# Kernel optimization log

Measured on AMD Instinct MI355X. Metric: run time of the kernel, lower is better.

Reference implementation:

```python
import jax, jax.numpy as jnp
import numpy as np

B, C, H, W = 32, 512, 64, 64
K = 32  # num_codes


def setup_inputs() -> dict:
    key = jax.random.key(0)
    k1, k2, k3 = jax.random.split(key, 3)
    x = jax.random.normal(k1, (B, C, H, W), dtype=jnp.float32)
    std = 1.0 / (K * C) ** 0.5
    codewords = jax.random.uniform(k2, (K, C), dtype=jnp.float32, minval=-std, maxval=std)
    scale = jax.random.uniform(k3, (K,), dtype=jnp.float32, minval=-1.0, maxval=0.0)
    return {"x": x, "codewords": codewords, "scale": scale}


def reference(x, codewords, scale):
    # x: [B, C, H, W] -> [B, N, C] with N = H*W
    b, c = x.shape[0], x.shape[1]
    xf = x.reshape(b, c, -1).transpose(0, 2, 1)  # [B, N, C]
    # scaled L2: scale_k * ||x_n - c_k||^2, expanded algebraically to avoid [B,N,K,C]
    x2 = jnp.sum(xf * xf, axis=-1)                      # [B, N]
    c2 = jnp.sum(codewords * codewords, axis=-1)        # [K]
    xc = jnp.einsum('bnc,kc->bnk', xf, codewords)       # [B, N, K]
    dist = scale[None, None, :] * (x2[:, :, None] - 2.0 * xc + c2[None, None, :])
    w = jax.nn.softmax(dist, axis=2)                    # [B, N, K]
    # aggregate: sum_n w_{nk} * (x_n - c_k) = (w^T x) - (sum_n w_{nk}) * c_k
    wx = jnp.einsum('bnk,bnc->bkc', w, xf)              # [B, K, C]
    wsum = jnp.sum(w, axis=1)                           # [B, K]
    encoded_feat = wx - wsum[:, :, None] * codewords[None, :, :]  # [B, K, C]
    return encoded_feat
```

## Files before the change

kernel.cpp:

```cpp
#include <hip/hip_runtime.h>
#include <hip/hip_bf16.h>
#include <stdint.h>

#define Bdim 32
#define Cdim 512
#define Ndim 4096
#define Kdim 32
#define NCHUNK 32
#define NCHUNKS 8
#define PBLK 16

static constexpr size_t WS_WSUM_OFF = (size_t)512 * Kdim * Cdim * 4;
static constexpr size_t WS_C2_OFF   = WS_WSUM_OFF + (size_t)512 * Kdim * 4;

typedef __fp16 hf2 __attribute__((ext_vector_type(2)));
typedef _Float16 ff2 __attribute__((ext_vector_type(2)));

static __device__ __forceinline__ float dot2f(hf2 a, hf2 b, float c) {
#if __has_builtin(__builtin_amdgcn_fdot2)
    return __builtin_amdgcn_fdot2(__builtin_bit_cast(ff2, a),
                                  __builtin_bit_cast(ff2, b), c, false);
#else
    return c + (float)a[0] * (float)b[0] + (float)a[1] * (float)b[1];
#endif
}

__global__ __launch_bounds__(256) void k0_c2(const float* __restrict__ cw,
                                             float* __restrict__ c2) {
    __shared__ float partl[8][32];
    int t = threadIdx.x;
    int k = t & 31, g = t >> 5;
    float s = 0.f;
    int c0 = g * 64;
    for (int c = c0; c < c0 + 64; ++c) {
        float v = cw[k * Cdim + c];
        s += v * v;
    }
    partl[g][k] = s;
    __syncthreads();
    if (t < 32) {
        float tot = 0.f;
        #pragma unroll
        for (int gg = 0; gg < 8; ++gg) tot += partl[gg][t];
        c2[t] = tot;
    }
}

__global__ __launch_bounds__(256, 2) void k1_fused(const float* __restrict__ x,
                                                   const float* __restrict__ cw,
                                                   const float* __restrict__ scale,
                                                   const float* __restrict__ c2g,
                                                   float* __restrict__ part,
                                                   float* __restrict__ wsum_part) {
    __shared__ hf2   xh[NCHUNK][260];
    __shared__ hf2   cwh[Kdim][256];
    __shared__ float w_s[NCHUNK][36];
    __shared__ float x2_s[NCHUNK];

    const int t   = threadIdx.x;
    const int blk = blockIdx.x;
    const int b   = blk >> 4;
    const int p   = blk & 15;

    const int n1 = t & 31;
    const int kq = t >> 5;
    const int q   = t & 7;
    const int cc0 = t >> 3;
    const int cg = t & 63;
    const int kh = t >> 6;

    float sc[4], cc2[4];
    #pragma unroll
    for (int j = 0; j < 4; ++j) {
        sc[j]  = scale[4 * kq + j];
        cc2[j] = c2g[4 * kq + j];
    }

    if (t < NCHUNK) x2_s[t] = 0.f;
    #pragma unroll
    for (int i = 0; i < 16; ++i) {
        int f4 = t + 256 * i;
        int k  = f4 >> 7;
        int c4 = f4 & 127;
        float4 v = *(const float4*)(cw + (size_t)k * Cdim + 4 * c4);
        cwh[k][2 * c4 + 0] = __builtin_amdgcn_cvt_pkrtz(v.x, v.y);
        cwh[k][2 * c4 + 1] = __builtin_amdgcn_cvt_pkrtz(v.z, v.w);
    }

    float acc[8][8];
    #pragma unroll
    for (int a = 0; a < 8; ++a)
        #pragma unroll
        for (int d = 0; d < 8; ++d) acc[a][d] = 0.f;
    float wsum_r = 0.f;

    const float* xb = x + (size_t)b * Cdim * Ndim + p * (NCHUNKS * NCHUNK);
    __syncthreads();

    for (int ci = 0; ci < NCHUNKS; ++ci) {
        const int n0 = ci * NCHUNK;

        float x2p[4] = {0.f, 0.f, 0.f, 0.f};
        #pragma unroll
        for (int it = 0; it < 8; ++it) {
            int cc = cc0 + 32 * it;
            const float* r0 = xb + (size_t)(2 * cc) * Ndim + n0 + 4 * q;
            float4 a  = *(const float4*)r0;
            float4 bb = *(const float4*)(r0 + Ndim);
            xh[4 * q + 0][cc] = __builtin_amdgcn_cvt_pkrtz(a.x, bb.x);
            xh[4 * q + 1][cc] = __builtin_amdgcn_cvt_pkrtz(a.y, bb.y);
            xh[4 * q + 2][cc] = __builtin_amdgcn_cvt_pkrtz(a.z, bb.z);
            xh[4 * q + 3][cc] = __builtin_amdgcn_cvt_pkrtz(a.w, bb.w);
            x2p[0] += a.x * a.x + bb.x * bb.x;
            x2p[1] += a.y * a.y + bb.y * bb.y;
            x2p[2] += a.z * a.z + bb.z * bb.z;
            x2p[3] += a.w * a.w + bb.w * bb.w;
        }
        #pragma unroll
        for (int j = 0; j < 4; ++j) {
            float v = x2p[j];
            v += __shfl_xor(v, 8);
            v += __shfl_xor(v, 16);
            v += __shfl_xor(v, 32);
            if ((t & 56) == 0) atomicAdd(&x2_s[4 * q + j], v);
        }
        __syncthreads();

        {
            const int k0 = 4 * kq;
            float d0 = 0.f, d1 = 0.f, d2 = 0.f, d3 = 0.f;
            #pragma unroll 4
            for (int cp = 0; cp < 64; ++cp) {
                uint4 xu = *(const uint4*)&xh[n1][4 * cp];
                hf2 x0 = __builtin_bit_cast(hf2, xu.x);
                hf2 x1 = __builtin_bit_cast(hf2, xu.y);
                hf2 x2v = __builtin_bit_cast(hf2, xu.z);
                hf2 x3 = __builtin_bit_cast(hf2, xu.w);
                uint4 cu0 = *(const uint4*)&cwh[k0 + 0][4 * cp];
                uint4 cu1 = *(const uint4*)&cwh[k0 + 1][4 * cp];
                uint4 cu2 = *(const uint4*)&cwh[k0 + 2][4 * cp];
                uint4 cu3 = *(const uint4*)&cwh[k0 + 3][4 * cp];
                d0 = dot2f(x0, __builtin_bit_cast(hf2, cu0.x), d0);
                d0 = dot2f(x1, __builtin_bit_cast(hf2, cu0.y), d0);
                d0 = dot2f(x2v, __builtin_bit_cast(hf2, cu0.z), d0);
                d0 = dot2f(x3, __builtin_bit_cast(hf2, cu0.w), d0);
                d1 = dot2f(x0, __builtin_bit_cast(hf2, cu1.x), d1);
                d1 = dot2f(x1, __builtin_bit_cast(hf2, cu1.y), d1);
                d1 = dot2f(x2v, __builtin_bit_cast(hf2, cu1.z), d1);
                d1 = dot2f(x3, __builtin_bit_cast(hf2, cu1.w), d1);
                d2 = dot2f(x0, __builtin_bit_cast(hf2, cu2.x), d2);
                d2 = dot2f(x1, __builtin_bit_cast(hf2, cu2.y), d2);
                d2 = dot2f(x2v, __builtin_bit_cast(hf2, cu2.z), d2);
                d2 = dot2f(x3, __builtin_bit_cast(hf2, cu2.w), d2);
                d3 = dot2f(x0, __builtin_bit_cast(hf2, cu3.x), d3);
                d3 = dot2f(x1, __builtin_bit_cast(hf2, cu3.y), d3);
                d3 = dot2f(x2v, __builtin_bit_cast(hf2, cu3.z), d3);
                d3 = dot2f(x3, __builtin_bit_cast(hf2, cu3.w), d3);
            }
            float xx = x2_s[n1];
            w_s[n1][k0 + 0] = sc[0] * (xx - 2.f * d0 + cc2[0]);
            w_s[n1][k0 + 1] = sc[1] * (xx - 2.f * d1 + cc2[1]);
            w_s[n1][k0 + 2] = sc[2] * (xx - 2.f * d2 + cc2[2]);
            w_s[n1][k0 + 3] = sc[3] * (xx - 2.f * d3 + cc2[3]);
        }
        __syncthreads();

        if (t < 32) {
            float v[32];
            float m = -3.4e38f;
            #pragma unroll
            for (int k = 0; k < 32; ++k) {
                v[k] = w_s[t][k];
                m = fmaxf(m, v[k]);
            }
            float s = 0.f;
            #pragma unroll
            for (int k = 0; k < 32; ++k) {
                v[k] = __expf(v[k] - m);
                s += v[k];
            }
            float inv = 1.f / s;
            #pragma unroll
            for (int k = 0; k < 32; ++k) w_s[t][k] = v[k] * inv;
        }
        __syncthreads();

        {
            const int k0 = 8 * kh;
            #pragma unroll 4
            for (int n = 0; n < NCHUNK; ++n) {
                uint4 xu = *(const uint4*)&xh[n][4 * cg];
                hf2 h0 = __builtin_bit_cast(hf2, xu.x);
                hf2 h1 = __builtin_bit_cast(hf2, xu.y);
                hf2 h2 = __builtin_bit_cast(hf2, xu.z);
                hf2 h3 = __builtin_bit_cast(hf2, xu.w);
                float xf[8];
                xf[0] = (float)h0[0]; xf[1] = (float)h0[1];
                xf[2] = (float)h1[0]; xf[3] = (float)h1[1];
                xf[4] = (float)h2[0]; xf[5] = (float)h2[1];
                xf[6] = (float)h3[0]; xf[7] = (float)h3[1];
                float4 wa = *(const float4*)&w_s[n][k0];
                float4 wb = *(const float4*)&w_s[n][k0 + 4];
                float wv[8] = {wa.x, wa.y, wa.z, wa.w, wb.x, wb.y, wb.z, wb.w};
                #pragma unroll
                for (int kk = 0; kk < 8; ++kk)
                    #pragma unroll
                    for (int j = 0; j < 8; ++j)
                        acc[kk][j] += wv[kk] * xf[j];
            }
        }
        if (t < 32) {
            float s = 0.f;
            #pragma unroll 4
            for (int n = 0; n < NCHUNK; ++n) s += w_s[n][t];
            wsum_r += s;
        } else if (t < 64) {
            x2_s[t - 32] = 0.f;
        }
        __syncthreads();
    }

    {
        const int k0 = 8 * kh;
        float* pb = part + (size_t)blk * (Kdim * Cdim);
        #pragma unroll
        for (int kk = 0; kk < 8; ++kk) {
            float4 v0 = make_float4(acc[kk][0], acc[kk][1], acc[kk][2], acc[kk][3]);
            float4 v1 = make_float4(acc[kk][4], acc[kk][5], acc[kk][6], acc[kk][7]);
            float* op = pb + (size_t)(k0 + kk) * Cdim + 8 * cg;
            *(float4*)op = v0;
            *(float4*)(op + 4) = v1;
        }
        if (t < 32) wsum_part[blk * Kdim + t] = wsum_r;
    }
}

__global__ __launch_bounds__(256) void k2_reduce(const float* __restrict__ part,
                                                 const float* __restrict__ wsum_part,
                                                 const float* __restrict__ cw,
                                                 float* __restrict__ out) {
    int blk = blockIdx.x;
    int b = blk >> 5, k = blk & 31;
    int t = threadIdx.x;
    float ws = 0.f;
    #pragma unroll
    for (int p = 0; p < PBLK; ++p) ws += wsum_part[(b * PBLK + p) * Kdim + k];
    int c = 2 * t;
    float sx = 0.f, sy = 0.f;
    #pragma unroll
    for (int p = 0; p < PBLK; ++p) {
        const float2 v = *(const float2*)(part + ((size_t)(b * PBLK + p) * Kdim + k) * Cdim + c);
        sx += v.x;
        sy += v.y;
    }
    float2 cv = *(const float2*)(cw + (size_t)k * Cdim + c);
    float2 o;
    o.x = sx - ws * cv.x;
    o.y = sy - ws * cv.y;
    *(float2*)(out + ((size_t)b * Kdim + k) * Cdim + c) = o;
}

extern "C" void kernel_launch(void* const* d_in, const int* in_sizes, int n_in,
                              void* d_out, int out_size, void* d_ws, size_t ws_size,
                              hipStream_t stream) {
    const float* x     = (const float*)d_in[0];
    const float* cw    = (const float*)d_in[1];
    const float* scale = (const float*)d_in[2];
    float* out = (float*)d_out;

    char* wsb = (char*)d_ws;
    float* part      = (float*)wsb;
    float* wsum_part = (float*)(wsb + WS_WSUM_OFF);
    float* c2        = (float*)(wsb + WS_C2_OFF);

    k0_c2<<<1, 256, 0, stream>>>(cw, c2);
    k1_fused<<<Bdim * PBLK, 256, 0, stream>>>(x, cw, scale, c2, part, wsum_part);
    k2_reduce<<<Bdim * Kdim, 256, 0, stream>>>(part, wsum_part, cw, out);
}
```

Measured before the change: 420.8 us.

## Rewrite fused encoding kernel with bf16 MFMA and register prefetch of next chunk

Replaces the fp16 dot2 distance computation and scalar FMA aggregation with bf16 MFMA 16x16x32 instructions for both the x·codeword and w^T·x products. The softmax is now spread across all 256 threads using shuffles instead of 32 threads. The next x chunk is prefetched into registers while the current one is processed. Blocks per batch drop from 16 to 8, with each block handling more pixels. bf16 inputs reduce precision compared to fp16, and having fewer blocks may leave some CUs underused.

```diff
diff --git a/kernel.cpp b/kernel.cpp
--- a/kernel.cpp
+++ b/kernel.cpp
@@ -1,28 +1,24 @@
 #include <hip/hip_runtime.h>
-#include <hip/hip_bf16.h>
 #include <stdint.h>
 
 #define Bdim 32
 #define Cdim 512
 #define Ndim 4096
 #define Kdim 32
-#define NCHUNK 32
-#define NCHUNKS 8
-#define PBLK 16
-
-static constexpr size_t WS_WSUM_OFF = (size_t)512 * Kdim * Cdim * 4;
-static constexpr size_t WS_C2_OFF   = WS_WSUM_OFF + (size_t)512 * Kdim * 4;
-
-typedef __fp16 hf2 __attribute__((ext_vector_type(2)));
-typedef _Float16 ff2 __attribute__((ext_vector_type(2)));
-
-static __device__ __forceinline__ float dot2f(hf2 a, hf2 b, float c) {
-#if __has_builtin(__builtin_amdgcn_fdot2)
-    return __builtin_amdgcn_fdot2(__builtin_bit_cast(ff2, a),
-                                  __builtin_bit_cast(ff2, b), c, false);
-#else
-    return c + (float)a[0] * (float)b[0] + (float)a[1] * (float)b[1];
-#endif
+#define NPX 32
+#define NCH 16
+#define PWIN 8
+
+static constexpr size_t WS_WSUM_OFF = (size_t)256 * Kdim * Cdim * 4;
+static constexpr size_t WS_C2_OFF   = WS_WSUM_OFF + (size_t)256 * Kdim * 4;
+
+using bf16x8 = __attribute__((ext_vector_type(8))) short;
+using f32x4  = __attribute__((ext_vector_type(4))) float;
+
+static __device__ __forceinline__ unsigned short f2bf(float f) {
+    unsigned int u = __float_as_uint(f);
+    u += 0x7fffu + ((u >> 16) & 1u);
+    return (unsigned short)(u >> 16);
 }
 
 __global__ __launch_bounds__(256) void k0_c2(const float* __restrict__ cw,
@@ -46,71 +42,84 @@
     }
 }
 
-__global__ __launch_bounds__(256, 2) void k1_fused(const float* __restrict__ x,
-                                                   const float* __restrict__ cw,
-                                                   const float* __restrict__ scale,
-                                                   const float* __restrict__ c2g,
-                                                   float* __restrict__ part,
-                                                   float* __restrict__ wsum_part) {
-    __shared__ hf2   xh[NCHUNK][260];
-    __shared__ hf2   cwh[Kdim][256];
-    __shared__ float w_s[NCHUNK][36];
-    __shared__ float x2_s[NCHUNK];
-
-    const int t   = threadIdx.x;
-    const int blk = blockIdx.x;
-    const int b   = blk >> 4;
-    const int p   = blk & 15;
-
-    const int n1 = t & 31;
-    const int kq = t >> 5;
-    const int q   = t & 7;
-    const int cc0 = t >> 3;
-    const int cg = t & 63;
-    const int kh = t >> 6;
-
-    float sc[4], cc2[4];
-    #pragma unroll
-    for (int j = 0; j < 4; ++j) {
-        sc[j]  = scale[4 * kq + j];
-        cc2[j] = c2g[4 * kq + j];
-    }
-
-    if (t < NCHUNK) x2_s[t] = 0.f;
+__global__ __launch_bounds__(256) void k1_fused(const float* __restrict__ x,
+                                                const float* __restrict__ cw,
+                                                const float* __restrict__ scale,
+                                                const float* __restrict__ c2g,
+                                                float* __restrict__ part,
+                                                float* __restrict__ wsum_part) {
+    __shared__ unsigned short cw_s[Kdim][520];
+    __shared__ unsigned short x_n[NPX][520];
+    __shared__ unsigned short x_t[Cdim][40];
+    __shared__ float          S_s[NPX][36];
+    __shared__ unsigned short w_t[Kdim][40];
+    __shared__ float          x2_s[NPX];
+    __shared__ float          wsum_s[Kdim];
+
+    const int t    = threadIdx.x;
+    const int blk  = blockIdx.x;
+    const int b    = blk >> 3;
+    const int pw   = blk & 7;
+    const int lane = t & 63;
+    const int lr   = lane & 15;
+    const int lq   = lane >> 4;
+    const int wv   = t >> 6;
+    const int q    = t & 7;
+    const int px   = t >> 3;
+
+    if (t < 32) { x2_s[t] = 0.f; wsum_s[t] = 0.f; }
+
     #pragma unroll
     for (int i = 0; i < 16; ++i) {
         int f4 = t + 256 * i;
         int k  = f4 >> 7;
-        int c4 = f4 & 127;
-        float4 v = *(const float4*)(cw + (size_t)k * Cdim + 4 * c4);
-        cwh[k][2 * c4 + 0] = __builtin_amdgcn_cvt_pkrtz(v.x, v.y);
-        cwh[k][2 * c4 + 1] = __builtin_amdgcn_cvt_pkrtz(v.z, v.w);
-    }
-
-    float acc[8][8];
-    #pragma unroll
-    for (int a = 0; a < 8; ++a)
-        #pragma unroll
-        for (int d = 0; d < 8; ++d) acc[a][d] = 0.f;
-    float wsum_r = 0.f;
-
-    const float* xb = x + (size_t)b * Cdim * Ndim + p * (NCHUNKS * NCHUNK);
+        int c4 = (f4 & 127) * 4;
+        float4 v = *(const float4*)(cw + (size_t)k * Cdim + c4);
+        ushort4 u;
+        u.x = f2bf(v.x); u.y = f2bf(v.y); u.z = f2bf(v.z); u.w = f2bf(v.w);
+        *(ushort4*)&cw_s[k][c4] = u;
+    }
+
+    const float4 sc4 = *(const float4*)(scale + 4 * q);
+    const float4 c24 = *(const float4*)(c2g + 4 * q);
+
+    const float* xb = x + (size_t)b * Cdim * Ndim;
+
+    float4 pa[8], pb[8];
+    {
+        int n0 = pw * 512;
+        #pragma unroll
+        for (int i = 0; i < 8; ++i) {
+            int c = 2 * px + 64 * i;
+            pa[i] = *(const float4*)(xb + (size_t)c * Ndim + n0 + 4 * q);
+            pb[i] = *(const float4*)(xb + (size_t)(c + 1) * Ndim + n0 + 4 * q);
+        }
+    }
+
+    f32x4 acc[2][8];
+    #pragma unroll
+    for (int kt = 0; kt < 2; ++kt)
+        #pragma unroll
+        for (int ct = 0; ct < 8; ++ct) acc[kt][ct] = (f32x4){0.f, 0.f, 0.f, 0.f};
+    float wsum_r[4] = {0.f, 0.f, 0.f, 0.f};
+
     __syncthreads();
 
-    for (int ci = 0; ci < NCHUNKS; ++ci) {
-        const int n0 = ci * NCHUNK;
-
+    for (int ci = 0; ci < NCH; ++ci) {
         float x2p[4] = {0.f, 0.f, 0.f, 0.f};
         #pragma unroll
-        for (int it = 0; it < 8; ++it) {
-            int cc = cc0 + 32 * it;
-            const float* r0 = xb + (size_t)(2 * cc) * Ndim + n0 + 4 * q;
-            float4 a  = *(const float4*)r0;
-            float4 bb = *(const float4*)(r0 + Ndim);
-            xh[4 * q + 0][cc] = __builtin_amdgcn_cvt_pkrtz(a.x, bb.x);
-            xh[4 * q + 1][cc] = __builtin_amdgcn_cvt_pkrtz(a.y, bb.y);
-            xh[4 * q + 2][cc] = __builtin_amdgcn_cvt_pkrtz(a.z, bb.z);
-            xh[4 * q + 3][cc] = __builtin_amdgcn_cvt_pkrtz(a.w, bb.w);
+        for (int i = 0; i < 8; ++i) {
+            int c = 2 * px + 64 * i;
+            float4 a = pa[i], bb = pb[i];
+            ushort4 ua, ub;
+            ua.x = f2bf(a.x);  ua.y = f2bf(a.y);  ua.z = f2bf(a.z);  ua.w = f2bf(a.w);
+            ub.x = f2bf(bb.x); ub.y = f2bf(bb.y); ub.z = f2bf(bb.z); ub.w = f2bf(bb.w);
+            *(ushort4*)&x_t[c][4 * q]     = ua;
+            *(ushort4*)&x_t[c + 1][4 * q] = ub;
+            ushort2 p0; p0.x = ua.x; p0.y = ub.x; *(ushort2*)&x_n[4 * q + 0][c] = p0;
+            ushort2 p1; p1.x = ua.y; p1.y = ub.y; *(ushort2*)&x_n[4 * q + 1][c] = p1;
+            ushort2 p2; p2.x = ua.z; p2.y = ub.z; *(ushort2*)&x_n[4 * q + 2][c] = p2;
+            ushort2 p3; p3.x = ua.w; p3.y = ub.w; *(ushort2*)&x_n[4 * q + 3][c] = p3;
             x2p[0] += a.x * a.x + bb.x * bb.x;
             x2p[1] += a.y * a.y + bb.y * bb.y;
             x2p[2] += a.z * a.z + bb.z * bb.z;
@@ -122,117 +131,98 @@
             v += __shfl_xor(v, 8);
             v += __shfl_xor(v, 16);
             v += __shfl_xor(v, 32);
-            if ((t & 56) == 0) atomicAdd(&x2_s[4 * q + j], v);
+            if (lane < 8) atomicAdd(&x2_s[4 * q + j], v);
+        }
+        if (ci + 1 < NCH) {
+            int nn = pw * 512 + (ci + 1) * 32;
+            #pragma unroll
+            for (int i = 0; i < 8; ++i) {
+                int c = 2 * px + 64 * i;
+                pa[i] = *(const float4*)(xb + (size_t)c * Ndim + nn + 4 * q);
+                pb[i] = *(const float4*)(xb + (size_t)(c + 1) * Ndim + nn + 4 * q);
+            }
         }
         __syncthreads();
 
         {
-            const int k0 = 4 * kq;
-            float d0 = 0.f, d1 = 0.f, d2 = 0.f, d3 = 0.f;
-            #pragma unroll 4
-            for (int cp = 0; cp < 64; ++cp) {
-                uint4 xu = *(const uint4*)&xh[n1][4 * cp];
-                hf2 x0 = __builtin_bit_cast(hf2, xu.x);
-                hf2 x1 = __builtin_bit_cast(hf2, xu.y);
-                hf2 x2v = __builtin_bit_cast(hf2, xu.z);
-                hf2 x3 = __builtin_bit_cast(hf2, xu.w);
-                uint4 cu0 = *(const uint4*)&cwh[k0 + 0][4 * cp];
-                uint4 cu1 = *(const uint4*)&cwh[k0 + 1][4 * cp];
-                uint4 cu2 = *(const uint4*)&cwh[k0 + 2][4 * cp];
-                uint4 cu3 = *(const uint4*)&cwh[k0 + 3][4 * cp];
-                d0 = dot2f(x0, __builtin_bit_cast(hf2, cu0.x), d0);
-                d0 = dot2f(x1, __builtin_bit_cast(hf2, cu0.y), d0);
-                d0 = dot2f(x2v, __builtin_bit_cast(hf2, cu0.z), d0);
-                d0 = dot2f(x3, __builtin_bit_cast(hf2, cu0.w), d0);
-                d1 = dot2f(x0, __builtin_bit_cast(hf2, cu1.x), d1);
-                d1 = dot2f(x1, __builtin_bit_cast(hf2, cu1.y), d1);
-                d1 = dot2f(x2v, __builtin_bit_cast(hf2, cu1.z), d1);
-                d1 = dot2f(x3, __builtin_bit_cast(hf2, cu1.w), d1);
-                d2 = dot2f(x0, __builtin_bit_cast(hf2, cu2.x), d2);
-                d2 = dot2f(x1, __builtin_bit_cast(hf2, cu2.y), d2);
-                d2 = dot2f(x2v, __builtin_bit_cast(hf2, cu2.z), d2);
-                d2 = dot2f(x3, __builtin_bit_cast(hf2, cu2.w), d2);
-                d3 = dot2f(x0, __builtin_bit_cast(hf2, cu3.x), d3);
-                d3 = dot2f(x1, __builtin_bit_cast(hf2, cu3.y), d3);
-                d3 = dot2f(x2v, __builtin_bit_cast(hf2, cu3.z), d3);
-                d3 = dot2f(x3, __builtin_bit_cast(hf2, cu3.w), d3);
+            const int pt = wv & 1, kt2 = wv >> 1;
+            f32x4 d = (f32x4){0.f, 0.f, 0.f, 0.f};
+            #pragma unroll
+            for (int s = 0; s < 16; ++s) {
+                bf16x8 av = *(const bf16x8*)&x_n[16 * pt + lr][32 * s + 8 * lq];
+                bf16x8 bv = *(const bf16x8*)&cw_s[16 * kt2 + lr][32 * s + 8 * lq];
+                d = __builtin_amdgcn_mfma_f32_16x16x32_bf16(av, bv, d, 0, 0, 0);
             }
-            float xx = x2_s[n1];
-            w_s[n1][k0 + 0] = sc[0] * (xx - 2.f * d0 + cc2[0]);
-            w_s[n1][k0 + 1] = sc[1] * (xx - 2.f * d1 + cc2[1]);
-            w_s[n1][k0 + 2] = sc[2] * (xx - 2.f * d2 + cc2[2]);
-            w_s[n1][k0 + 3] = sc[3] * (xx - 2.f * d3 + cc2[3]);
-        }
-        __syncthreads();
-
-        if (t < 32) {
-            float v[32];
-            float m = -3.4e38f;
-            #pragma unroll
-            for (int k = 0; k < 32; ++k) {
-                v[k] = w_s[t][k];
-                m = fmaxf(m, v[k]);
+            #pragma unroll
+            for (int r = 0; r < 4; ++r)
+                S_s[16 * pt + 4 * lq + r][16 * kt2 + lr] = d[r];
+        }
+        __syncthreads();
+
+        {
+            float4 dv = *(const float4*)&S_s[px][4 * q];
+            float xx = x2_s[px];
+            float d0 = sc4.x * (xx - 2.f * dv.x + c24.x);
+            float d1 = sc4.y * (xx - 2.f * dv.y + c24.y);
+            float d2 = sc4.z * (xx - 2.f * dv.z + c24.z);
+            float d3 = sc4.w * (xx - 2.f * dv.w + c24.w);
+            float m = fmaxf(fmaxf(d0, d1), fmaxf(d2, d3));
+            m = fmaxf(m, __shfl_xor(m, 1));
+            m = fmaxf(m, __shfl_xor(m, 2));
+            m = fmaxf(m, __shfl_xor(m, 4));
+            float e0 = __expf(d0 - m), e1 = __expf(d1 - m);
+            float e2 = __expf(d2 - m), e3 = __expf(d3 - m);
+            float ss = e0 + e1 + e2 + e3;
+            ss += __shfl_xor(ss, 1);
+            ss += __shfl_xor(ss, 2);
+            ss += __shfl_xor(ss, 4);
+            float inv = 1.f / ss;
+            float w0 = e0 * inv, w1 = e1 * inv, w2 = e2 * inv, w3 = e3 * inv;
+            wsum_r[0] += w0; wsum_r[1] += w1; wsum_r[2] += w2; wsum_r[3] += w3;
+            w_t[4 * q + 0][px] = f2bf(w0);
+            w_t[4 * q + 1][px] = f2bf(w1);
+            w_t[4 * q + 2][px] = f2bf(w2);
+            w_t[4 * q + 3][px] = f2bf(w3);
+        }
+        __syncthreads();
+
+        {
+            const int c0w = 128 * wv;
+            bf16x8 a0 = *(const bf16x8*)&w_t[lr][8 * lq];
+            bf16x8 a1 = *(const bf16x8*)&w_t[16 + lr][8 * lq];
+            if (t < 32) x2_s[t] = 0.f;
+            #pragma unroll
+            for (int ct = 0; ct < 8; ++ct) {
+                bf16x8 bv = *(const bf16x8*)&x_t[c0w + 16 * ct + lr][8 * lq];
+                acc[0][ct] = __builtin_amdgcn_mfma_f32_16x16x32_bf16(a0, bv, acc[0][ct], 0, 0, 0);
+                acc[1][ct] = __builtin_amdgcn_mfma_f32_16x16x32_bf16(a1, bv, acc[1][ct], 0, 0, 0);
             }
-            float s = 0.f;
-            #pragma unroll
-            for (int k = 0; k < 32; ++k) {
-                v[k] = __expf(v[k] - m);
-                s += v[k];
-            }
-            float inv = 1.f / s;
-            #pragma unroll
-            for (int k = 0; k < 32; ++k) w_s[t][k] = v[k] * inv;
-        }
-        __syncthreads();
-
-        {
-            const int k0 = 8 * kh;
-            #pragma unroll 4
-            for (int n = 0; n < NCHUNK; ++n) {
-                uint4 xu = *(const uint4*)&xh[n][4 * cg];
-                hf2 h0 = __builtin_bit_cast(hf2, xu.x);
-                hf2 h1 = __builtin_bit_cast(hf2, xu.y);
-                hf2 h2 = __builtin_bit_cast(hf2, xu.z);
-                hf2 h3 = __builtin_bit_cast(hf2, xu.w);
-                float xf[8];
-                xf[0] = (float)h0[0]; xf[1] = (float)h0[1];
-                xf[2] = (float)h1[0]; xf[3] = (float)h1[1];
-                xf[4] = (float)h2[0]; xf[5] = (float)h2[1];
-                xf[6] = (float)h3[0]; xf[7] = (float)h3[1];
-                float4 wa = *(const float4*)&w_s[n][k0];
-                float4 wb = *(const float4*)&w_s[n][k0 + 4];
-                float wv[8] = {wa.x, wa.y, wa.z, wa.w, wb.x, wb.y, wb.z, wb.w};
+        }
+        __syncthreads();
+    }
+
+    #pragma unroll
+    for (int j = 0; j < 4; ++j) {
+        float v = wsum_r[j];
+        v += __shfl_xor(v, 8);
+        v += __shfl_xor(v, 16);
+        v += __shfl_xor(v, 32);
+        if (lane < 8) atomicAdd(&wsum_s[4 * q + j], v);
+    }
+    {
+        const int c0w = 128 * wv;
+        float* pbuf = part + (size_t)blk * (Kdim * Cdim);
+        #pragma unroll
+        for (int kt = 0; kt < 2; ++kt)
+            #pragma unroll
+            for (int ct = 0; ct < 8; ++ct)
                 #pragma unroll
-                for (int kk = 0; kk < 8; ++kk)
-                    #pragma unroll
-                    for (int j = 0; j < 8; ++j)
-                        acc[kk][j] += wv[kk] * xf[j];
-            }
-        }
-        if (t < 32) {
-            float s = 0.f;
-            #pragma unroll 4
-            for (int n = 0; n < NCHUNK; ++n) s += w_s[n][t];
-            wsum_r += s;
-        } else if (t < 64) {
-            x2_s[t - 32] = 0.f;
-        }
-        __syncthreads();
-    }
-
-    {
-        const int k0 = 8 * kh;
-        float* pb = part + (size_t)blk * (Kdim * Cdim);
-        #pragma unroll
-        for (int kk = 0; kk < 8; ++kk) {
-            float4 v0 = make_float4(acc[kk][0], acc[kk][1], acc[kk][2], acc[kk][3]);
-            float4 v1 = make_float4(acc[kk][4], acc[kk][5], acc[kk][6], acc[kk][7]);
-            float* op = pb + (size_t)(k0 + kk) * Cdim + 8 * cg;
-            *(float4*)op = v0;
-            *(float4*)(op + 4) = v1;
-        }
-        if (t < 32) wsum_part[blk * Kdim + t] = wsum_r;
-    }
+                for (int r = 0; r < 4; ++r)
+                    pbuf[(size_t)(16 * kt + 4 * lq + r) * Cdim + c0w + 16 * ct + lr] =
+                        acc[kt][ct][r];
+    }
+    __syncthreads();
+    if (t < 32) wsum_part[blk * Kdim + t] = wsum_s[t];
 }
 
 __global__ __launch_bounds__(256) void k2_reduce(const float* __restrict__ part,
@@ -244,12 +234,12 @@
     int t = threadIdx.x;
     float ws = 0.f;
     #pragma unroll
-    for (int p = 0; p < PBLK; ++p) ws += wsum_part[(b * PBLK + p) * Kdim + k];
+    for (int p = 0; p < PWIN; ++p) ws += wsum_part[(b * PWIN + p) * Kdim + k];
     int c = 2 * t;
     float sx = 0.f, sy = 0.f;
     #pragma unroll
-    for (int p = 0; p < PBLK; ++p) {
-        const float2 v = *(const float2*)(part + ((size_t)(b * PBLK + p) * Kdim + k) * Cdim + c);
+    for (int p = 0; p < PWIN; ++p) {
+        const float2 v = *(const float2*)(part + ((size_t)(b * PWIN + p) * Kdim + k) * Cdim + c);
         sx += v.x;
         sy += v.y;
     }
@@ -274,6 +264,6 @@
     float* c2        = (float*)(wsb + WS_C2_OFF);
 
     k0_c2<<<1, 256, 0, stream>>>(cw, c2);
-    k1_fused<<<Bdim * PBLK, 256, 0, stream>>>(x, cw, scale, c2, part, wsum_part);
+    k1_fused<<<Bdim * PWIN, 256, 0, stream>>>(x, cw, scale, c2, part, wsum_part);
     k2_reduce<<<Bdim * Kdim, 256, 0, stream>>>(part, wsum_part, cw, out);
 }
```

New measurement: 384.4 us. -8.6%, faster.
